# Kernel optimization log

Hardware: AMD Instinct MI355X
Metric: run time of the kernel (lower is better)

The kernel has to match this reference:

```python
import jax, jax.numpy as jnp
import numpy as np

DIM = 1024; VOCAB = 32000; HEADS = 16; HEAD_DIM = DIM // HEADS
SEG = 128; NPT = 16; WIDTH = 128
THETA = 0.1; ETA = 0.9; ALPHA = 0.01; EPS = 1e-6  # neural-memory lr / momentum / weight-decay


def l2n(x):
    return x / (jnp.linalg.norm(x, axis=-1, keepdims=True) + EPS)


def mlp(p, x):
    # 2-layer memory MLP: dim -> width -> dim, SiLU
    W1, b1, W2, b2 = p
    return jax.nn.silu(x @ W1 + b1) @ W2 + b2


def setup_inputs() -> dict:
    key = jax.random.key(0)
    ks = jax.random.split(key, 12)
    g = lambda k, s: jax.random.normal(k, s, jnp.float32) * 0.02
    z = lambda n: jnp.zeros((n,), jnp.float32)
    return {
        "x": jax.random.randint(ks[0], (2, 512), 0, VOCAB),
        "embedding": g(ks[1], (VOCAB, DIM)),
        "persistent": g(ks[2], (NPT, DIM)),
        "Wq": g(ks[3], (DIM, DIM)), "bq": z(DIM),
        "Wk": g(ks[4], (DIM, DIM)), "bk": z(DIM),
        "Wv": g(ks[5], (DIM, DIM)), "bv": z(DIM),
        "attn_in_w": g(ks[6], (DIM, 3 * DIM)), "attn_in_b": z(3 * DIM),
        "attn_out_w": g(ks[7], (DIM, DIM)), "attn_out_b": z(DIM),
        "mW1": g(ks[8], (DIM, WIDTH)), "mb1": z(WIDTH),
        "mW2": g(ks[9], (WIDTH, DIM)), "mb2": z(DIM),
        "head_w": g(ks[10], (DIM, VOCAB)), "head_b": z(VOCAB),
    }


def reference(x, embedding, persistent, Wq, bq, Wk, bk, Wv, bv,
              attn_in_w, attn_in_b, attn_out_w, attn_out_b,
              mW1, mb1, mW2, mb2, head_w, head_b):
    B, N = x.shape
    x_emb = embedding[x]  # [B, N, D]
    pad = (-N) % SEG
    if pad:
        x_emb = jnp.pad(x_emb, ((0, 0), (0, pad), (0, 0)))
    S = x_emb.shape[1] // SEG
    segs = x_emb.reshape(B, S, SEG, DIM).transpose(1, 0, 2, 3)  # [S, B, L, D]

    T = NPT + 2 * SEG  # persistent + retrieved memory + segment tokens
    causal = jnp.triu(jnp.ones((T, T), bool), 1)

    def mha(xc):  # [B, T, D] -> [B, T, D], torch nn.MultiheadAttention math
        q, k, v = jnp.split(xc @ attn_in_w + attn_in_b, 3, axis=-1)
        split = lambda t: t.reshape(B, T, HEADS, HEAD_DIM).transpose(0, 2, 1, 3)
        q, k, v = split(q), split(k), split(v)
        scores = jnp.einsum('bhqd,bhkd->bhqk', q, k) / np.sqrt(HEAD_DIM).astype(np.float32)
        scores = jnp.where(causal, -jnp.inf, scores)
        out = jnp.einsum('bhqk,bhkd->bhqd', jax.nn.softmax(scores, axis=-1), v)
        return out.transpose(0, 2, 1, 3).reshape(B, T, DIM) @ attn_out_w + attn_out_b

    # per-sample memory params (leading B axis) + zero momentum
    params0 = tuple(jnp.broadcast_to(w, (B,) + w.shape) for w in (mW1, mb1, mW2, mb2))
    mom0 = tuple(jnp.zeros_like(p) for p in params0)

    def mem_loss(p, k, v):
        e = mlp(p, k) - v
        return jnp.sum(e * e)

    def tok_step(carry, tok):  # tok: [B, D] -- one test-time gradient step on memory
        p, m = carry
        k = jax.lax.stop_gradient(l2n(tok @ Wk + bk))  # stop_grad_k=True
        v = tok @ Wv + bv                               # stop_grad_v=False
        grads = jax.vmap(jax.grad(mem_loss))(p, k, v)
        m = jax.tree.map(lambda mm, g: ETA * mm - THETA * g, m, grads)
        p = jax.tree.map(lambda pp, mm: (1.0 - ALPHA) * pp + mm, p, m)
        return (p, m), None

    retrieve = jax.vmap(mlp)  # vmap over per-sample memory params

    def seg_step(carry, segment):  # segment: [B, L, D]
        p, m = carry
        h = retrieve(p, l2n(segment @ Wq + bq))
        combined = jnp.concatenate(
            [jnp.broadcast_to(persistent, (B, NPT, DIM)), h, segment], axis=1)
        seg_out = mha(combined)[:, -SEG:, :]
        (p, m), _ = jax.lax.scan(tok_step, (p, m), seg_out.transpose(1, 0, 2))
        mem_out = retrieve(p, l2n(seg_out @ Wq + bq))
        return (p, m), seg_out * mem_out

    _, outs = jax.lax.scan(seg_step, (params0, mom0), segs)  # outs: [S, B, L, D]
    full = outs.transpose(1, 0, 2, 3).reshape(B, S * SEG, DIM)[:, :N, :]
    return full @ head_w + head_b
```

## Files before the change

kernel.cpp:

```cpp
#include <hip/hip_runtime.h>
#include <math.h>

#define D_    1024
#define B_    2
#define N_    512
#define SEG_  128
#define NSEG_ 4
#define NPT_  16
#define T_    272
#define NH_   16
#define HD_   64
#define W_    128
#define V_    32000

#define THETA_ 0.1f
#define ETA_   0.9f
#define PDEC_  0.99f
#define EPSN_  1e-6f
#define NB2_  32
#define FSTR_ 32

typedef __bf16 bf16x8 __attribute__((ext_vector_type(8)));
typedef float  f32x4  __attribute__((ext_vector_type(4)));

static const size_t XEMB = 0;
static const size_t OUTS = XEMB + (size_t)B_*N_*D_;
static const size_t PW1  = OUTS + (size_t)B_*N_*D_;
static const size_t PB1  = PW1  + (size_t)B_*D_*W_;
static const size_t PW2T = PB1  + (size_t)B_*W_;
static const size_t PB2  = PW2T + (size_t)B_*D_*W_;
static const size_t MOM  = PB2  + (size_t)B_*D_;
static const size_t MW1  = MOM;
static const size_t MB1  = MW1  + (size_t)B_*D_*W_;
static const size_t MW2T = MB1  + (size_t)B_*W_;
static const size_t MB2  = MW2T + (size_t)B_*D_*W_;
static const size_t MOMSZ = (size_t)B_*(D_*W_ + W_ + D_*W_ + D_);
static const size_t Q1   = MOM  + MOMSZ;
static const size_t AH   = Q1   + (size_t)B_*SEG_*D_;
static const size_t HBUF = AH   + (size_t)B_*SEG_*W_;
static const size_t COMB = HBUF + (size_t)B_*SEG_*D_;
static const size_t QKV  = COMB + (size_t)B_*T_*D_;
static const size_t ATTN = QKV  + (size_t)B_*T_*3*D_;
static const size_t SEGO = ATTN + (size_t)B_*SEG_*D_;
static const size_t KM   = SEGO + (size_t)B_*SEG_*D_;
static const size_t VM   = KM   + (size_t)B_*SEG_*D_;
static const size_t MEMO = VM   + (size_t)B_*SEG_*D_;
static const size_t WSEND = MEMO + (size_t)B_*SEG_*D_;

static const size_t AQ1K  = QKV;
static const size_t AQ1KM = AQ1K  + 32768;
static const size_t AGRAM = AQ1KM + 32768;
static const size_t ADZ1  = AGRAM + 32768;
static const size_t AA1H  = ADZ1  + 32768;
static const size_t AEH   = AA1H  + 32768;
static const size_t AEXR  = AEH + (size_t)B_*SEG_*D_;
static const size_t AEXEE = AEXR + 16384;
static const size_t COEF  = WSEND;
static const size_t ZEROB = COEF + 512;
static const size_t CBAR  = ZEROB + 128;

__device__ __forceinline__ float sigf(float x) { return 1.f/(1.f+expf(-x)); }

__device__ __forceinline__ void gstore(float* p, float v) {
  __hip_atomic_store(p, v, __ATOMIC_RELAXED, __HIP_MEMORY_SCOPE_AGENT);
}
__device__ __forceinline__ float gload(const float* p) {
  return __hip_atomic_load(p, __ATOMIC_RELAXED, __HIP_MEMORY_SCOPE_AGENT);
}

__device__ __forceinline__ void bsplit(float a, short& h, short& l) {
  unsigned u = __builtin_bit_cast(unsigned, a);
  unsigned hb = (u + 0x7fffu + ((u >> 16) & 1u)) >> 16;
  h = (short)hb;
  float hf = __builtin_bit_cast(float, hb << 16);
  float r = a - hf;
  unsigned ur = __builtin_bit_cast(unsigned, r);
  unsigned lb = (ur + 0x7fffu + ((ur >> 16) & 1u)) >> 16;
  l = (short)lb;
}

template<int BT, int SILU>
__global__ __launch_bounds__(256) void k_gemm(
    const float* __restrict__ A, const float* __restrict__ Bm,
    const float* __restrict__ bias, float* __restrict__ C,
    int M, int N, int K, long sA, long sB, long sC, long sBias)
{
  __shared__ float As[16][68];
  __shared__ float Bs[16][68];
  int bz = blockIdx.z;
  A += bz*sA; Bm += bz*sB; C += bz*sC; bias += bz*sBias;
  int n0 = blockIdx.x*64, m0 = blockIdx.y*64;
  int tid = threadIdx.x;
  int tx = tid & 15, ty = tid >> 4;
  int r  = tid >> 2;
  int kq = (tid & 3) * 4;
  float acc[4][4] = {};
  for (int k0 = 0; k0 < K; k0 += 16) {
    {
      int row = m0 + r;
      float4 v = make_float4(0.f,0.f,0.f,0.f);
      if (row < M) v = *(const float4*)(A + (long)row*K + k0 + kq);
      As[kq+0][r]=v.x; As[kq+1][r]=v.y; As[kq+2][r]=v.z; As[kq+3][r]=v.w;
    }
    if (BT) {
      int row = n0 + r;
      float4 v = *(const float4*)(Bm + (long)row*K + k0 + kq);
      Bs[kq+0][r]=v.x; Bs[kq+1][r]=v.y; Bs[kq+2][r]=v.z; Bs[kq+3][r]=v.w;
    } else {
      int c = tid & 63, r4 = tid >> 6;
      #pragma unroll
      for (int p = 0; p < 4; p++) {
        int kk = r4 + p*4;
        Bs[kk][c] = Bm[(long)(k0+kk)*N + n0 + c];
      }
    }
    __syncthreads();
    #pragma unroll
    for (int kk = 0; kk < 16; kk++) {
      float av[4], bv[4];
      #pragma unroll
      for (int i=0;i<4;i++) av[i] = As[kk][ty*4+i];
      #pragma unroll
      for (int j=0;j<4;j++) bv[j] = Bs[kk][tx*4+j];
      #pragma unroll
      for (int i=0;i<4;i++)
        #pragma unroll
        for (int j=0;j<4;j++)
          acc[i][j] = fmaf(av[i], bv[j], acc[i][j]);
    }
    __syncthreads();
  }
  #pragma unroll
  for (int i=0;i<4;i++) {
    int row = m0 + ty*4 + i;
    if (row >= M) continue;
    #pragma unroll
    for (int j=0;j<4;j++) {
      int col = n0 + tx*4 + j;
      float v = acc[i][j] + bias[col];
      if (SILU) v = v * sigf(v);
      C[(long)row*N + col] = v;
    }
  }
}

__global__ __launch_bounds__(256) void k_gemm2(
    const float* __restrict__ A, const float* __restrict__ B1,
    const float* __restrict__ B2, float* __restrict__ C1, float* __restrict__ C2,
    int K, long sA, long sB, long sC)
{
  __shared__ float As[16][68];
  __shared__ float B1s[16][68];
  __shared__ float B2s[16][68];
  int bz = blockIdx.z;
  A += bz*sA; B1 += bz*sB; B2 += bz*sB; C1 += bz*sC; C2 += bz*sC;
  int n0 = blockIdx.x*64, m0 = blockIdx.y*64;
  int tid = threadIdx.x;
  int tx = tid & 15, ty = tid >> 4;
  int r  = tid >> 2;
  int kq = (tid & 3) * 4;
  float acc1[4][4] = {}, acc2[4][4] = {};
  for (int k0 = 0; k0 < K; k0 += 16) {
    {
      float4 v = *(const float4*)(A + (long)(m0+r)*K + k0 + kq);
      As[kq+0][r]=v.x; As[kq+1][r]=v.y; As[kq+2][r]=v.z; As[kq+3][r]=v.w;
    }
    {
      int c = tid & 63, r4 = tid >> 6;
      #pragma unroll
      for (int p = 0; p < 4; p++) {
        int kk = r4 + p*4;
        B1s[kk][c] = B1[(long)(k0+kk)*W_ + n0 + c];
        B2s[kk][c] = B2[(long)(k0+kk)*W_ + n0 + c];
      }
    }
    __syncthreads();
    #pragma unroll
    for (int kk = 0; kk < 16; kk++) {
      float av[4], b1v[4], b2v[4];
      #pragma unroll
      for (int i=0;i<4;i++) av[i] = As[kk][ty*4+i];
      #pragma unroll
      for (int j=0;j<4;j++) { b1v[j] = B1s[kk][tx*4+j]; b2v[j] = B2s[kk][tx*4+j]; }
      #pragma unroll
      for (int i=0;i<4;i++)
        #pragma unroll
        for (int j=0;j<4;j++) {
          acc1[i][j] = fmaf(av[i], b1v[j], acc1[i][j]);
          acc2[i][j] = fmaf(av[i], b2v[j], acc2[i][j]);
        }
    }
    __syncthreads();
  }
  #pragma unroll
  for (int i=0;i<4;i++) {
    int row = m0 + ty*4 + i;
    #pragma unroll
    for (int j=0;j<4;j++) {
      int col = n0 + tx*4 + j;
      C1[(long)row*W_ + col] = acc1[i][j];
      C2[(long)row*W_ + col] = acc2[i][j];
    }
  }
}

__global__ __launch_bounds__(256) void k_gemm128(
    const float* __restrict__ A, const float* __restrict__ Bm,
    const float* __restrict__ bias, float* __restrict__ C,
    int M, int N, int K)
{
  __shared__ float As[16][132];
  __shared__ float Bs[16][132];
  int n0 = blockIdx.x*128, m0 = blockIdx.y*128;
  int tid = threadIdx.x;
  int tx = tid & 15, ty = tid >> 4;
  int ar = tid >> 1, ak = (tid & 1) * 8;
  int bk = tid >> 4, bn = (tid & 15) * 8;
  int arow = min(m0 + ar, M-1);
  float acc[8][8] = {};
  for (int k0 = 0; k0 < K; k0 += 16) {
    {
      const float* ap = A + (long)arow*K + k0 + ak;
      float4 v0 = *(const float4*)(ap);
      float4 v1 = *(const float4*)(ap+4);
      As[ak+0][ar]=v0.x; As[ak+1][ar]=v0.y; As[ak+2][ar]=v0.z; As[ak+3][ar]=v0.w;
      As[ak+4][ar]=v1.x; As[ak+5][ar]=v1.y; As[ak+6][ar]=v1.z; As[ak+7][ar]=v1.w;
      const float* bp = Bm + (long)(k0+bk)*N + n0 + bn;
      *(float4*)(&Bs[bk][bn])   = *(const float4*)(bp);
      *(float4*)(&Bs[bk][bn+4]) = *(const float4*)(bp+4);
    }
    __syncthreads();
    #pragma unroll
    for (int kk = 0; kk < 16; kk++) {
      float av[8], bv[8];
      #pragma unroll
      for (int i=0;i<8;i++) av[i] = As[kk][ty*8+i];
      #pragma unroll
      for (int j=0;j<8;j++) bv[j] = Bs[kk][tx*8+j];
      #pragma unroll
      for (int i=0;i<8;i++)
        #pragma unroll
        for (int j=0;j<8;j++)
          acc[i][j] = fmaf(av[i], bv[j], acc[i][j]);
    }
    __syncthreads();
  }
  #pragma unroll
  for (int i=0;i<8;i++) {
    int row = m0 + ty*8 + i;
    if (row >= M) continue;
    #pragma unroll
    for (int j=0;j<8;j++) acc[i][j] += bias[n0 + tx*8 + j];
    *(float4*)(C + (long)row*N + n0 + tx*8)     = make_float4(acc[i][0],acc[i][1],acc[i][2],acc[i][3]);
    *(float4*)(C + (long)row*N + n0 + tx*8 + 4) = make_float4(acc[i][4],acc[i][5],acc[i][6],acc[i][7]);
  }
}

__global__ __launch_bounds__(256) void k_head_mfma(
    const float* __restrict__ A, const float* __restrict__ Bm,
    const float* __restrict__ bias, float* __restrict__ C,
    int M, int N, int K)
{
  __shared__ short Ah[128][48];
  __shared__ short Al[128][48];
  __shared__ short Bh[32][132];
  __shared__ short Bl[32][132];
  int n0 = blockIdx.x*128, m0 = blockIdx.y*128;
  int tid = threadIdx.x;
  int wave = tid >> 6, lane = tid & 63;
  int wm = (wave >> 1) * 64, wn = (wave & 1) * 64;
  int lrow = lane & 15, lk = (lane >> 4) * 8;
  f32x4 acc[4][4] = {};
  for (int k0 = 0; k0 < K; k0 += 32) {
    __syncthreads();
    {
      int r = tid >> 1, kq = (tid & 1) * 16;
      const float* ap = A + (long)(m0 + r)*K + k0 + kq;
      #pragma unroll
      for (int q = 0; q < 16; q += 4) {
        float4 v = *(const float4*)(ap + q);
        short h0,l0,h1,l1,h2,l2,h3,l3;
        bsplit(v.x,h0,l0); bsplit(v.y,h1,l1); bsplit(v.z,h2,l2); bsplit(v.w,h3,l3);
        *(short4*)&Ah[r][kq+q] = make_short4(h0,h1,h2,h3);
        *(short4*)&Al[r][kq+q] = make_short4(l0,l1,l2,l3);
      }
    }
    {
      int kr = tid >> 3, nq = (tid & 7) * 16;
      const float* bp = Bm + (long)(k0 + kr)*N + n0 + nq;
      #pragma unroll
      for (int q = 0; q < 16; q += 4) {
        float4 v = *(const float4*)(bp + q);
        short h0,l0,h1,l1,h2,l2,h3,l3;
        bsplit(v.x,h0,l0); bsplit(v.y,h1,l1); bsplit(v.z,h2,l2); bsplit(v.w,h3,l3);
        *(short4*)&Bh[kr][nq+q] = make_short4(h0,h1,h2,h3);
        *(short4*)&Bl[kr][nq+q] = make_short4(l0,l1,l2,l3);
      }
    }
    __syncthreads();
    bf16x8 bh[4], bl[4];
    #pragma unroll
    for (int nf = 0; nf < 4; nf++) {
      int col = wn + nf*16 + lrow;
      #pragma unroll
      for (int j = 0; j < 8; j++) {
        bh[nf][j] = __builtin_bit_cast(__bf16, Bh[lk+j][col]);
        bl[nf][j] = __builtin_bit_cast(__bf16, Bl[lk+j][col]);
      }
    }
    #pragma unroll
    for (int mf = 0; mf < 4; mf++) {
      int arow2 = wm + mf*16 + lrow;
      bf16x8 ah = *(const bf16x8*)&Ah[arow2][lk];
      bf16x8 al = *(const bf16x8*)&Al[arow2][lk];
      #pragma unroll
      for (int nf = 0; nf < 4; nf++) {
        acc[mf][nf] = __builtin_amdgcn_mfma_f32_16x16x32_bf16(ah, bh[nf], acc[mf][nf], 0, 0, 0);
        acc[mf][nf] = __builtin_amdgcn_mfma_f32_16x16x32_bf16(ah, bl[nf], acc[mf][nf], 0, 0, 0);
        acc[mf][nf] = __builtin_amdgcn_mfma_f32_16x16x32_bf16(al, bh[nf], acc[mf][nf], 0, 0, 0);
      }
    }
  }
  #pragma unroll
  for (int mf = 0; mf < 4; mf++) {
    #pragma unroll
    for (int nf = 0; nf < 4; nf++) {
      int col = n0 + wn + nf*16 + lrow;
      float bv = bias[col];
      #pragma unroll
      for (int j = 0; j < 4; j++) {
        int row = m0 + wm + mf*16 + (lane >> 4)*4 + j;
        C[(long)row*N + col] = acc[mf][nf][j] + bv;
      }
    }
  }
}

__global__ void k_embed(const int* __restrict__ x, const float* __restrict__ emb,
                        float* __restrict__ xe)
{
  int row = blockIdx.x, tid = threadIdx.x;
  int idx = x[row];
  float4 v = *(const float4*)(emb + (long)idx*D_ + tid*4);
  *(float4*)(xe + (long)row*D_ + tid*4) = v;
}

#define PER_ 263296L
__global__ void k_init(const float* __restrict__ mW1in, const float* __restrict__ mb1in,
                       const float* __restrict__ mW2in, const float* __restrict__ mb2in,
                       float* __restrict__ pW1, float* __restrict__ pb1,
                       float* __restrict__ pW2T, float* __restrict__ pb2)
{
  long g = (long)blockIdx.x*256 + threadIdx.x;
  if (g >= 2*PER_) return;
  int b = (int)(g / PER_);
  long rr = g % PER_;
  if (rr < 131072)       pW1[(long)b*131072 + rr] = mW1in[rr];
  else if (rr < 131200)  pb1[b*W_ + (rr-131072)] = mb1in[rr-131072];
  else if (rr < 262272) { long l = rr-131200; int j=(int)(l>>7), h=(int)(l&127);
                          pW2T[(long)b*131072 + l] = mW2in[(long)h*D_ + j]; }
  else                   pb2[b*D_ + (rr-262272)] = mb2in[rr-262272];
}

__global__ void k_coef(float* __restrict__ c)
{
  if (blockIdx.x == 0 && threadIdx.x == 0) {
    c[0] = 1.f; c[128] = 1.f;
    float A = 1.f, eta_d = 1.f;
    for (int d = 1; d < 128; d++) {
      eta_d *= ETA_;
      A = PDEC_*A + eta_d;
      c[d] = A;
      c[128 + d] = eta_d;
    }
    c[256] = 1.f;
    float bp = 1.f;
    for (int t = 1; t <= 128; t++) { bp *= PDEC_; c[256 + t] = bp; }
  }
}

__global__ __launch_bounds__(256) void k_l2n(float* __restrict__ X)
{
  long row = blockIdx.x;
  float* p = X + row*D_;
  int tid = threadIdx.x;
  float4 v = *(float4*)(p + tid*4);
  float ss = v.x*v.x + v.y*v.y + v.z*v.z + v.w*v.w;
  for (int o=32;o;o>>=1) ss += __shfl_xor(ss,o);
  __shared__ float wsum[4];
  if ((tid&63)==0) wsum[tid>>6] = ss;
  __syncthreads();
  float tot = wsum[0]+wsum[1]+wsum[2]+wsum[3];
  float sc = 1.f/(sqrtf(tot)+EPSN_);
  v.x*=sc; v.y*=sc; v.z*=sc; v.w*=sc;
  *(float4*)(p + tid*4) = v;
}

__global__ void k_concat(const float* __restrict__ pers, const float* __restrict__ h,
                         const float* __restrict__ xemb, int s, float* __restrict__ comb)
{
  int row = blockIdx.x, b = blockIdx.y, tid = threadIdx.x;
  const float* src;
  if (row < NPT_)            src = pers + (long)row*D_;
  else if (row < NPT_+SEG_)  src = h    + ((long)b*SEG_ + (row-NPT_))*D_;
  else                       src = xemb + ((long)b*N_ + s*SEG_ + (row-NPT_-SEG_))*D_;
  float4 v = *(const float4*)(src + tid*4);
  *(float4*)(comb + ((long)b*T_ + row)*D_ + tid*4) = v;
}

__global__ __launch_bounds__(256) void k_attn(const float* __restrict__ qkv,
                                              float* __restrict__ outp)
{
  __shared__ float sQ[16][68];
  __shared__ float sKV[64][68];
  __shared__ float sS[16][273];
  int qt = blockIdx.x, head = blockIdx.y, b = blockIdx.z;
  int tid = threadIdx.x;
  const float* base = qkv + (long)b*T_*3*D_;
  int qoff = head*HD_, koff = D_ + head*HD_, voff = 2*D_ + head*HD_;
  int qrow0 = NPT_ + SEG_ + qt*16;
  {
    int rr = tid>>4, c4 = (tid&15)*4;
    float4 v = *(const float4*)(base + (long)(qrow0+rr)*3*D_ + qoff + c4);
    sQ[rr][c4]=v.x; sQ[rr][c4+1]=v.y; sQ[rr][c4+2]=v.z; sQ[rr][c4+3]=v.w;
  }
  __syncthreads();
  for (int j0 = 0; j0 < T_; j0 += 64) {
    int chunk = min(64, T_ - j0);
    {
      int jj = tid>>2, cq = (tid&3)*16;
      if (jj < chunk) {
        #pragma unroll
        for (int q4=0;q4<4;q4++) {
          float4 v = *(const float4*)(base + (long)(j0+jj)*3*D_ + koff + cq + q4*4);
          sKV[jj][cq+q4*4]=v.x; sKV[jj][cq+q4*4+1]=v.y; sKV[jj][cq+q4*4+2]=v.z; sKV[jj][cq+q4*4+3]=v.w;
        }
      }
    }
    __syncthreads();
    int rr = tid>>4, jj0 = tid&15;
    #pragma unroll
    for (int p=0;p<4;p++) {
      int jj = jj0 + p*16;
      if (jj < chunk) {
        float s = 0.f;
        #pragma unroll 8
        for (int c=0;c<HD_;c++) s = fmaf(sQ[rr][c], sKV[jj][c], s);
        s *= 0.125f;
        int jg = j0 + jj, qg = qrow0 + rr;
        if (jg > qg) s = -3.0e38f;
        sS[rr][jg] = s;
      }
    }
    __syncthreads();
  }
  {
    int rr = tid>>4, l16 = tid&15;
    float m = -3.4e38f;
    for (int j=l16; j<T_; j+=16) m = fmaxf(m, sS[rr][j]);
    for (int o=8;o;o>>=1) m = fmaxf(m, __shfl_xor(m,o));
    float sum = 0.f;
    for (int j=l16; j<T_; j+=16) { float e = expf(sS[rr][j]-m); sS[rr][j] = e; sum += e; }
    for (int o=8;o;o>>=1) sum += __shfl_xor(sum,o);
    float inv = 1.f/sum;
    for (int j=l16; j<T_; j+=16) sS[rr][j] *= inv;
  }
  __syncthreads();
  float acc[4] = {0.f,0.f,0.f,0.f};
  int rr = tid>>4, c4 = (tid&15)*4;
  for (int j0 = 0; j0 < T_; j0 += 64) {
    int chunk = min(64, T_ - j0);
    {
      int jj = tid>>2, cq = (tid&3)*16;
      if (jj < chunk) {
        #pragma unroll
        for (int q4=0;q4<4;q4++) {
          float4 v = *(const float4*)(base + (long)(j0+jj)*3*D_ + voff + cq + q4*4);
          sKV[jj][cq+q4*4]=v.x; sKV[jj][cq+q4*4+1]=v.y; sKV[jj][cq+q4*4+2]=v.z; sKV[jj][cq+q4*4+3]=v.w;
        }
      }
    }
    __syncthreads();
    for (int jj=0; jj<chunk; jj++) {
      float p = sS[rr][j0+jj];
      #pragma unroll
      for (int i=0;i<4;i++) acc[i] = fmaf(p, sKV[jj][c4+i], acc[i]);
    }
    __syncthreads();
  }
  float4 o4 = make_float4(acc[0],acc[1],acc[2],acc[3]);
  *(float4*)(outp + ((long)(b*SEG_) + qt*16 + rr)*D_ + head*HD_ + c4) = o4;
}

__device__ __forceinline__ void gbar(int* flags, int blk, int gen)
{
  asm volatile("s_waitcnt vmcnt(0) lgkmcnt(0)" ::: "memory");
  __syncthreads();
  if (threadIdx.x == 0)
    __hip_atomic_store(flags + blk*FSTR_, gen, __ATOMIC_RELAXED, __HIP_MEMORY_SCOPE_AGENT);
  if (threadIdx.x < NB2_) {
    while (__hip_atomic_load(flags + threadIdx.x*FSTR_, __ATOMIC_RELAXED,
                             __HIP_MEMORY_SCOPE_AGENT) < gen)
      __builtin_amdgcn_s_sleep(1);
  }
  __syncthreads();
}

__global__ __launch_bounds__(256) void k_scan(
  const float* __restrict__ pW2T, const float* __restrict__ mW2T,
  float* __restrict__ pb1, float* __restrict__ mb1,
  float* __restrict__ pb2, float* __restrict__ mb2,
  const float* __restrict__ Vm,
  const float* __restrict__ q1k, const float* __restrict__ q1km,
  const float* __restrict__ G,
  float* __restrict__ dz1o, float* __restrict__ a1o, float* __restrict__ eo,
  float* __restrict__ exR, float* __restrict__ exEE,
  const float* __restrict__ coef, int* __restrict__ barbase, int seg)
{
  __shared__ float sDZ[128][129];
  __shared__ float sA1[128][129];
  __shared__ float sEh[128][33];
  __shared__ float sB1[128], sMB1[128], sZ1[128], sR[128];
  __shared__ float sB2[32], sMB2[32];
  __shared__ float sAt[128];
  __shared__ float sBp[129];
  __shared__ float sGc[128];
  __shared__ float sS[128];
  __shared__ float sEEc[128];

  int b = blockIdx.y, blk = blockIdx.x, tid = threadIdx.x;
  int j0 = blk*32;
  int* flags = barbase + b*(NB2_*FSTR_);
  int gbase = seg*200;
  const float* W0 = pW2T + (long)b*131072;
  const float* Wm = mW2T + (long)b*131072;

  if (tid < 128) { sAt[tid] = coef[tid]; sB1[tid] = pb1[b*W_+tid]; sMB1[tid] = mb1[b*W_+tid]; }
  else if (tid < 160) { int j = tid-128; sB2[j] = pb2[b*D_+j0+j]; sMB2[j] = mb2[b*D_+j0+j]; }
  for (int i = tid; i < 129; i += 256) sBp[i] = coef[256+i];
  __syncthreads();

  for (int t = 0; t < SEG_; ++t) {
    int par = t & 1;
    float bp = sBp[t];
    float ca = (t>0) ? ETA_*sAt[t-1] : 0.f;

    float rq1k = 0.f, rq1km = 0.f;
    if (tid < 128) {
      rq1k  = q1k [((long)b*SEG_+t)*W_ + tid];
      rq1km = q1km[((long)b*SEG_+t)*W_ + tid];
      if (t > 0) {
        float mm = ETA_*sMB1[tid] - THETA_*sDZ[t-1][tid];
        sMB1[tid] = mm; sB1[tid] = PDEC_*sB1[tid] + mm;
      }
      if (tid < t) sGc[tid] = sAt[t-1-tid]*G[((long)b*SEG_+t)*SEG_ + tid];
    } else if (tid < 160) {
      int j = tid-128;
      if (t > 0) {
        float mm = ETA_*sMB2[j] - 2.f*THETA_*sEh[t-1][j];
        sMB2[j] = mm; sB2[j] = PDEC_*sB2[j] + mm;
      }
    }
    __syncthreads();

    if (tid < 128) {
      float acc = 0.f;
      for (int u = 0; u < t; ++u) acc = fmaf(sGc[u], sDZ[u][tid], acc);
      float z1 = bp*rq1k + ca*rq1km + sB1[tid] - THETA_*acc;
      sZ1[tid] = z1;
      sA1[t][tid] = z1 * sigf(z1);
    }
    __syncthreads();

    if (tid < t) {
      float acc = 0.f;
      #pragma unroll 8
      for (int h = 0; h < 128; ++h) acc = fmaf(sA1[tid][h], sA1[t][h], acc);
      sS[tid] = -2.f*THETA_*sAt[t-1-tid]*acc;
    }
    __syncthreads();

    {
      int j = tid >> 3, l = tid & 7;
      const float* w0r = W0 + (long)(j0+j)*128;
      const float* wmr = Wm + (long)(j0+j)*128;
      float g = 0.f, gm = 0.f;
      for (int h = l; h < 128; h += 8) {
        g  = fmaf(w0r[h], sA1[t][h], g);
        gm = fmaf(wmr[h], sA1[t][h], gm);
      }
      float corr = 0.f;
      for (int u = l; u < t; u += 8) corr = fmaf(sS[u], sEh[u][j], corr);
      float tot = bp*g + ca*gm + corr;
      tot += __shfl_xor(tot,4); tot += __shfl_xor(tot,2); tot += __shfl_xor(tot,1);
      if (l == 0) sEh[t][j] = tot + sB2[j] - Vm[((long)b*SEG_+t)*D_ + j0+j];
    }
    __syncthreads();

    {
      int h = tid >> 1, half = tid & 1;
      float racc = 0.f;
      for (int jj = half*16; jj < half*16+16; ++jj) {
        float w = bp*W0[(long)(j0+jj)*128 + h] + ca*Wm[(long)(j0+jj)*128 + h];
        racc = fmaf(w, sEh[t][jj], racc);
      }
      racc += __shfl_xor(racc,1);
      if (half == 0) gstore(&exR[(((long)par*B_ + b)*NB2_ + blk)*W_ + h], racc);
      if (h < t) {
        float eacc = 0.f;
        for (int jj = half*16; jj < half*16+16; ++jj)
          eacc = fmaf(sEh[h][jj], sEh[t][jj], eacc);
        eacc += __shfl_xor(eacc,1);
        if (half == 0) gstore(&exEE[(((long)par*B_ + b)*NB2_ + blk)*W_ + h], eacc);
      }
    }
    gbar(flags, blk, gbase + t + 1);

    {
      int h = tid >> 1, half = tid & 1;
      float racc = 0.f;
      #pragma unroll
      for (int k = 0; k < 16; ++k)
        racc += gload(&exR[(((long)par*B_ + b)*NB2_ + half*16 + k)*W_ + h]);
      racc += __shfl_xor(racc,1);
      if (half == 0) sR[h] = racc;
      if (h < t) {
        float eacc = 0.f;
        #pragma unroll
        for (int k = 0; k < 16; ++k)
          eacc += gload(&exEE[(((long)par*B_ + b)*NB2_ + half*16 + k)*W_ + h]);
        eacc += __shfl_xor(eacc,1);
        if (half == 0) sEEc[h] = -2.f*THETA_*sAt[t-1-h]*eacc;
      }
    }
    __syncthreads();
    if (tid < 128) {
      float macc = 0.f;
      for (int u = 0; u < t; ++u) macc = fmaf(sEEc[u], sA1[u][tid], macc);
      float z = sZ1[tid], sg = sigf(z);
      sDZ[t][tid] = 2.f*(sR[tid] + macc)*sg*(1.f + z*(1.f - sg));
    }
    __syncthreads();
  }

  if (tid < 128) {
    if (blk == 0) {
      float mm = ETA_*sMB1[tid] - THETA_*sDZ[127][tid];
      mb1[b*W_ + tid] = mm;
      pb1[b*W_ + tid] = PDEC_*sB1[tid] + mm;
    }
  } else if (tid < 160) {
    int j = tid-128;
    float mm = ETA_*sMB2[j] - 2.f*THETA_*sEh[127][j];
    mb2[b*D_ + j0+j] = mm;
    pb2[b*D_ + j0+j] = PDEC_*sB2[j] + mm;
  }
  for (int i = tid; i < 128*4; i += 256) {
    int t2 = i >> 2, hh = (i & 3) + blk*4;
    dz1o[((long)b*SEG_+t2)*W_ + hh] = sDZ[t2][hh];
    a1o [((long)b*SEG_+t2)*W_ + hh] = sA1[t2][hh];
  }
  for (int i = tid; i < 128*32; i += 256) {
    int t2 = i >> 5, jj = i & 31;
    eo[((long)b*SEG_+t2)*D_ + j0+jj] = sEh[t2][jj];
  }
}

__global__ __launch_bounds__(256) void k_recon(
  float* __restrict__ pW1, float* __restrict__ mW1,
  float* __restrict__ pW2T, float* __restrict__ mW2T,
  const float* __restrict__ KMp, const float* __restrict__ Eh,
  const float* __restrict__ DZ1, const float* __restrict__ A1h,
  const float* __restrict__ coef)
{
  __shared__ float s1[16][33];
  __shared__ float s2[16][65];
  __shared__ float sCA[128], sCE[128];
  int dt = blockIdx.x, ht = blockIdx.y, kb = blockIdx.z;
  int kind = kb >> 1, b = kb & 1;
  int tid = threadIdx.x;
  int d0 = dt*32, hb = ht*64;
  const float* in1 = (kind ? Eh : KMp) + (long)b*SEG_*D_;
  const float* in2 = (kind ? A1h : DZ1) + (long)b*SEG_*W_;
  float* Pb = (kind ? pW2T : pW1) + (long)b*131072;
  float* Mb = (kind ? mW2T : mW1) + (long)b*131072;
  float f = kind ? -2.f*THETA_ : -THETA_;
  if (tid < 128) {
    sCA[tid] = f*coef[127 - tid];
    sCE[tid] = f*coef[128 + 127 - tid];
  }
  __syncthreads();
  int dd = tid >> 3, le = tid & 7;
  float accP[8] = {}, accM[8] = {};
  for (int u0 = 0; u0 < 128; u0 += 16) {
    for (int i = tid; i < 16*32; i += 256) {
      int uu = i >> 5, d2 = i & 31;
      s1[uu][d2] = in1[(long)(u0+uu)*D_ + d0 + d2];
    }
    for (int i = tid; i < 16*64; i += 256) {
      int uu = i >> 6, hl = i & 63;
      s2[uu][hl] = in2[(long)(u0+uu)*W_ + hb + hl];
    }
    __syncthreads();
    #pragma unroll
    for (int uu = 0; uu < 16; uu++) {
      float a = s1[uu][dd];
      float cAu = sCA[u0+uu], cEu = sCE[u0+uu];
      #pragma unroll
      for (int k = 0; k < 8; k++) {
        float v = a * s2[uu][k*8 + le];
        accP[k] = fmaf(cAu, v, accP[k]);
        accM[k] = fmaf(cEu, v, accM[k]);
      }
    }
    __syncthreads();
  }
  float b128 = coef[256 + 128];
  float eA   = ETA_*coef[127];
  float e128 = ETA_*coef[128 + 127];
  #pragma unroll
  for (int k = 0; k < 8; k++) {
    long idx = (long)(d0+dd)*W_ + hb + k*8 + le;
    float Po = Pb[idx], Mo = Mb[idx];
    Pb[idx] = b128*Po + eA*Mo + accP[k];
    Mb[idx] = e128*Mo + accM[k];
  }
}

__global__ __launch_bounds__(256) void k_gemmkvq(
    const float* __restrict__ A,
    const float* __restrict__ Wk, const float* __restrict__ bk,
    const float* __restrict__ Wv, const float* __restrict__ bv,
    const float* __restrict__ Wq, const float* __restrict__ bq,
    float* __restrict__ KMo, float* __restrict__ VMo, float* __restrict__ Q1o)
{
  __shared__ float As[16][132];
  __shared__ float Bs[16][132];
  int bx = blockIdx.x;
  int sel = bx >> 3;
  int c0 = (bx & 7) * 128;
  int m0 = blockIdx.y * 128;
  const float* Bm   = sel == 0 ? Wk : sel == 1 ? Wv : Wq;
  const float* bias = sel == 0 ? bk : sel == 1 ? bv : bq;
  float* C          = sel == 0 ? KMo : sel == 1 ? VMo : Q1o;
  int tid = threadIdx.x;
  int tx = tid & 15, ty = tid >> 4;
  int ar = tid >> 1, ak = (tid & 1) * 8;
  int bkr = tid >> 4, bn = (tid & 15) * 8;
  float acc[8][8] = {};
  for (int k0 = 0; k0 < D_; k0 += 16) {
    {
      const float* ap = A + (long)(m0+ar)*D_ + k0 + ak;
      float4 v0 = *(const float4*)(ap);
      float4 v1 = *(const float4*)(ap+4);
      As[ak+0][ar]=v0.x; As[ak+1][ar]=v0.y; As[ak+2][ar]=v0.z; As[ak+3][ar]=v0.w;
      As[ak+4][ar]=v1.x; As[ak+5][ar]=v1.y; As[ak+6][ar]=v1.z; As[ak+7][ar]=v1.w;
      const float* bp = Bm + (long)(k0+bkr)*D_ + c0 + bn;
      *(float4*)(&Bs[bkr][bn])   = *(const float4*)(bp);
      *(float4*)(&Bs[bkr][bn+4]) = *(const float4*)(bp+4);
    }
    __syncthreads();
    #pragma unroll
    for (int kk = 0; kk < 16; kk++) {
      float av[8], bv8[8];
      #pragma unroll
      for (int i=0;i<8;i++) av[i] = As[kk][ty*8+i];
      #pragma unroll
      for (int j=0;j<8;j++) bv8[j] = Bs[kk][tx*8+j];
      #pragma unroll
      for (int i=0;i<8;i++)
        #pragma unroll
        for (int j=0;j<8;j++)
          acc[i][j] = fmaf(av[i], bv8[j], acc[i][j]);
    }
    __syncthreads();
  }
  #pragma unroll
  for (int i=0;i<8;i++) {
    int row = m0 + ty*8 + i;
    #pragma unroll
    for (int j=0;j<8;j++) acc[i][j] += bias[c0 + tx*8 + j];
    *(float4*)(C + (long)row*D_ + c0 + tx*8)     = make_float4(acc[i][0],acc[i][1],acc[i][2],acc[i][3]);
    *(float4*)(C + (long)row*D_ + c0 + tx*8 + 4) = make_float4(acc[i][4],acc[i][5],acc[i][6],acc[i][7]);
  }
}

__global__ void k_mul(const float* __restrict__ so, const float* __restrict__ mo,
                      float* __restrict__ outs, int s)
{
  int l = blockIdx.x, b = blockIdx.y, tid = threadIdx.x;
  long src = ((long)b*SEG_ + l)*D_ + tid*4;
  float4 a = *(const float4*)(so + src);
  float4 c = *(const float4*)(mo + src);
  a.x*=c.x; a.y*=c.y; a.z*=c.z; a.w*=c.w;
  *(float4*)(outs + ((long)b*N_ + s*SEG_ + l)*D_ + tid*4) = a;
}

static inline void gemm(const float* A, const float* Bm, const float* bias, float* C,
                        int M, int N, int K, long sA, long sB, long sC, long sBias,
                        int batch, int bt, int silu_, hipStream_t st)
{
  dim3 g(N/64, (M+63)/64, batch), blk(256);
  if (!bt && !silu_) k_gemm<0,0><<<g,blk,0,st>>>(A,Bm,bias,C,M,N,K,sA,sB,sC,sBias);
  else if (!bt && silu_) k_gemm<0,1><<<g,blk,0,st>>>(A,Bm,bias,C,M,N,K,sA,sB,sC,sBias);
  else k_gemm<1,0><<<g,blk,0,st>>>(A,Bm,bias,C,M,N,K,sA,sB,sC,sBias);
}

extern "C" void kernel_launch(void* const* d_in, const int* in_sizes, int n_in,
                              void* d_out, int out_size, void* d_ws, size_t ws_size,
                              hipStream_t stream)
{
  (void)in_sizes; (void)n_in; (void)out_size; (void)ws_size;
  const int*   x     = (const int*)  d_in[0];
  const float* emb   = (const float*)d_in[1];
  const float* pers  = (const float*)d_in[2];
  const float* Wq    = (const float*)d_in[3];
  const float* bq    = (const float*)d_in[4];
  const float* Wk    = (const float*)d_in[5];
  const float* bk    = (const float*)d_in[6];
  const float* Wv    = (const float*)d_in[7];
  const float* bv    = (const float*)d_in[8];
  const float* aiw   = (const float*)d_in[9];
  const float* aib   = (const float*)d_in[10];
  const float* aow   = (const float*)d_in[11];
  const float* aob   = (const float*)d_in[12];
  const float* mW1in = (const float*)d_in[13];
  const float* mb1in = (const float*)d_in[14];
  const float* mW2in = (const float*)d_in[15];
  const float* mb2in = (const float*)d_in[16];
  const float* headw = (const float*)d_in[17];
  const float* headb = (const float*)d_in[18];
  float* out = (float*)d_out;
  float* ws  = (float*)d_ws;

  hipMemsetAsync(ws + MOM, 0, MOMSZ*sizeof(float), stream);
  hipMemsetAsync(ws + ZEROB, 0, 128*sizeof(float), stream);
  hipMemsetAsync(ws + CBAR, 0, (size_t)B_*NB2_*FSTR_*sizeof(int), stream);
  k_embed<<<dim3(B_*N_), dim3(256), 0, stream>>>(x, emb, ws+XEMB);
  k_init<<<dim3((2*PER_+255)/256), dim3(256), 0, stream>>>(
      mW1in, mb1in, mW2in, mb2in, ws+PW1, ws+PB1, ws+PW2T, ws+PB2);
  k_coef<<<dim3(1), dim3(64), 0, stream>>>(ws+COEF);

  for (int s = 0; s < NSEG_; s++) {
    const float* segA = ws + XEMB + (size_t)s*SEG_*D_;
    gemm(segA, Wq, bq, ws+Q1, SEG_, D_, D_, (long)N_*D_, 0, (long)SEG_*D_, 0, B_, 0, 0, stream);
    k_l2n<<<dim3(B_*SEG_), dim3(256), 0, stream>>>(ws+Q1);
    gemm(ws+Q1, ws+PW1, ws+PB1, ws+AH, SEG_, W_, D_, (long)SEG_*D_, (long)D_*W_, (long)SEG_*W_, W_, B_, 0, 1, stream);
    gemm(ws+AH, ws+PW2T, ws+PB2, ws+HBUF, SEG_, D_, W_, (long)SEG_*W_, (long)D_*W_, (long)SEG_*D_, D_, B_, 1, 0, stream);
    k_concat<<<dim3(T_, B_), dim3(256), 0, stream>>>(pers, ws+HBUF, ws+XEMB, s, ws+COMB);
    k_gemm128<<<dim3(3*D_/128, (B_*T_+127)/128), dim3(256), 0, stream>>>(
        ws+COMB, aiw, aib, ws+QKV, B_*T_, 3*D_, D_);
    k_attn<<<dim3(8, NH_, B_), dim3(256), 0, stream>>>(ws+QKV, ws+ATTN);
    gemm(ws+ATTN, aow, aob, ws+SEGO, B_*SEG_, D_, D_, 0, 0, 0, 0, 1, 0, 0, stream);
    k_gemmkvq<<<dim3(24, 2), dim3(256), 0, stream>>>(
        ws+SEGO, Wk, bk, Wv, bv, Wq, bq, ws+KM, ws+VM, ws+Q1);
    k_l2n<<<dim3(B_*SEG_), dim3(256), 0, stream>>>(ws+KM);
    k_l2n<<<dim3(B_*SEG_), dim3(256), 0, stream>>>(ws+Q1);
    k_gemm2<<<dim3(2, 2, B_), dim3(256), 0, stream>>>(
        ws+KM, ws+PW1, ws+MW1, ws+AQ1K, ws+AQ1KM,
        D_, (long)SEG_*D_, (long)D_*W_, (long)SEG_*W_);
    gemm(ws+KM, ws+KM,  ws+ZEROB, ws+AGRAM, SEG_, SEG_, D_, (long)SEG_*D_, (long)SEG_*D_, (long)SEG_*SEG_, 0, B_, 1, 0, stream);
    k_scan<<<dim3(NB2_, B_), dim3(256), 0, stream>>>(
        ws+PW2T, ws+MW2T, ws+PB1, ws+MB1, ws+PB2, ws+MB2, ws+VM,
        ws+AQ1K, ws+AQ1KM, ws+AGRAM,
        ws+ADZ1, ws+AA1H, ws+AEH,
        ws+AEXR, ws+AEXEE,
        ws+COEF, (int*)(ws+CBAR), s);
    k_recon<<<dim3(32, 2, 4), dim3(256), 0, stream>>>(
        ws+PW1, ws+MW1, ws+PW2T, ws+MW2T,
        ws+KM, ws+AEH, ws+ADZ1, ws+AA1H, ws+COEF);
    gemm(ws+Q1, ws+PW1, ws+PB1, ws+AH, SEG_, W_, D_, (long)SEG_*D_, (long)D_*W_, (long)SEG_*W_, W_, B_, 0, 1, stream);
    gemm(ws+AH, ws+PW2T, ws+PB2, ws+MEMO, SEG_, D_, W_, (long)SEG_*W_, (long)D_*W_, (long)SEG_*D_, D_, B_, 1, 0, stream);
    k_mul<<<dim3(SEG_, B_), dim3(256), 0, stream>>>(ws+SEGO, ws+MEMO, ws+OUTS, s);
  }
  k_head_mfma<<<dim3(V_/128, (B_*N_)/128), dim3(256), 0, stream>>>(
      ws+OUTS, headw, headb, out, B_*N_, V_, D_);
}
```

Before: 8.503 ms.

## Move dense projections to split-bf16 MFMA and cache scan weights in registers

Replaces the FP32 SIMT tiled GEMMs for the Wq projection, QKV in-projection, attention out-projection and fused K/V/Q projection with a bf16 MFMA kernel. Each FP32 operand is split into high and low bf16 parts and three MFMA products are accumulated to stay close to FP32 accuracy. The sequential per-token scan kernel now preloads its slice of the W2 parameter and momentum rows into registers once, instead of re-reading them from global memory on every token step. The split-bf16 path trades some precision and extra MFMA work for matrix-core throughput, and the register cache raises register pressure in the scan kernel.

New measurement: 7.426 ms. -12.7%, faster.

```diff
diff --git a/kernel.cpp b/kernel.cpp
--- a/kernel.cpp
+++ b/kernel.cpp
@@ -204,55 +204,174 @@
   }
 }
 
-__global__ __launch_bounds__(256) void k_gemm128(
+__global__ __launch_bounds__(256) void k_gemm_mfma(
     const float* __restrict__ A, const float* __restrict__ Bm,
     const float* __restrict__ bias, float* __restrict__ C,
-    int M, int N, int K)
-{
-  __shared__ float As[16][132];
-  __shared__ float Bs[16][132];
+    int M, int N, int K, long sA, long sB, long sC, long sBias)
+{
+  __shared__ short Ah[128][48];
+  __shared__ short Al[128][48];
+  __shared__ short Bh[32][132];
+  __shared__ short Bl[32][132];
+  int bz = blockIdx.z;
+  A += bz*sA; Bm += bz*sB; C += bz*sC; bias += bz*sBias;
   int n0 = blockIdx.x*128, m0 = blockIdx.y*128;
   int tid = threadIdx.x;
-  int tx = tid & 15, ty = tid >> 4;
-  int ar = tid >> 1, ak = (tid & 1) * 8;
-  int bk = tid >> 4, bn = (tid & 15) * 8;
-  int arow = min(m0 + ar, M-1);
-  float acc[8][8] = {};
-  for (int k0 = 0; k0 < K; k0 += 16) {
-    {
-      const float* ap = A + (long)arow*K + k0 + ak;
-      float4 v0 = *(const float4*)(ap);
-      float4 v1 = *(const float4*)(ap+4);
-      As[ak+0][ar]=v0.x; As[ak+1][ar]=v0.y; As[ak+2][ar]=v0.z; As[ak+3][ar]=v0.w;
-      As[ak+4][ar]=v1.x; As[ak+5][ar]=v1.y; As[ak+6][ar]=v1.z; As[ak+7][ar]=v1.w;
-      const float* bp = Bm + (long)(k0+bk)*N + n0 + bn;
-      *(float4*)(&Bs[bk][bn])   = *(const float4*)(bp);
-      *(float4*)(&Bs[bk][bn+4]) = *(const float4*)(bp+4);
-    }
-    __syncthreads();
-    #pragma unroll
-    for (int kk = 0; kk < 16; kk++) {
-      float av[8], bv[8];
-      #pragma unroll
-      for (int i=0;i<8;i++) av[i] = As[kk][ty*8+i];
-      #pragma unroll
-      for (int j=0;j<8;j++) bv[j] = Bs[kk][tx*8+j];
-      #pragma unroll
-      for (int i=0;i<8;i++)
-        #pragma unroll
-        for (int j=0;j<8;j++)
-          acc[i][j] = fmaf(av[i], bv[j], acc[i][j]);
-    }
-    __syncthreads();
+  int wave = tid >> 6, lane = tid & 63;
+  int wm = (wave >> 1) * 64, wn = (wave & 1) * 64;
+  int lrow = lane & 15, lk = (lane >> 4) * 8;
+  int arow0 = min(m0 + (tid >> 1), M-1);
+  f32x4 acc[4][4] = {};
+  for (int k0 = 0; k0 < K; k0 += 32) {
+    __syncthreads();
+    {
+      int r = tid >> 1, kq = (tid & 1) * 16;
+      const float* ap = A + (long)arow0*K + k0 + kq;
+      #pragma unroll
+      for (int q = 0; q < 16; q += 4) {
+        float4 v = *(const float4*)(ap + q);
+        short h0,l0,h1,l1,h2,l2,h3,l3;
+        bsplit(v.x,h0,l0); bsplit(v.y,h1,l1); bsplit(v.z,h2,l2); bsplit(v.w,h3,l3);
+        *(short4*)&Ah[r][kq+q] = make_short4(h0,h1,h2,h3);
+        *(short4*)&Al[r][kq+q] = make_short4(l0,l1,l2,l3);
+      }
+    }
+    {
+      int kr = tid >> 3, nq = (tid & 7) * 16;
+      const float* bp = Bm + (long)(k0 + kr)*N + n0 + nq;
+      #pragma unroll
+      for (int q = 0; q < 16; q += 4) {
+        float4 v = *(const float4*)(bp + q);
+        short h0,l0,h1,l1,h2,l2,h3,l3;
+        bsplit(v.x,h0,l0); bsplit(v.y,h1,l1); bsplit(v.z,h2,l2); bsplit(v.w,h3,l3);
+        *(short4*)&Bh[kr][nq+q] = make_short4(h0,h1,h2,h3);
+        *(short4*)&Bl[kr][nq+q] = make_short4(l0,l1,l2,l3);
+      }
+    }
+    __syncthreads();
+    bf16x8 bh[4], bl[4];
+    #pragma unroll
+    for (int nf = 0; nf < 4; nf++) {
+      int col = wn + nf*16 + lrow;
+      #pragma unroll
+      for (int j = 0; j < 8; j++) {
+        bh[nf][j] = __builtin_bit_cast(__bf16, Bh[lk+j][col]);
+        bl[nf][j] = __builtin_bit_cast(__bf16, Bl[lk+j][col]);
+      }
+    }
+    #pragma unroll
+    for (int mf = 0; mf < 4; mf++) {
+      int ar2 = wm + mf*16 + lrow;
+      bf16x8 ah = *(const bf16x8*)&Ah[ar2][lk];
+      bf16x8 al = *(const bf16x8*)&Al[ar2][lk];
+      #pragma unroll
+      for (int nf = 0; nf < 4; nf++) {
+        acc[mf][nf] = __builtin_amdgcn_mfma_f32_16x16x32_bf16(ah, bh[nf], acc[mf][nf], 0, 0, 0);
+        acc[mf][nf] = __builtin_amdgcn_mfma_f32_16x16x32_bf16(ah, bl[nf], acc[mf][nf], 0, 0, 0);
+        acc[mf][nf] = __builtin_amdgcn_mfma_f32_16x16x32_bf16(al, bh[nf], acc[mf][nf], 0, 0, 0);
+      }
+    }
   }
   #pragma unroll
-  for (int i=0;i<8;i++) {
-    int row = m0 + ty*8 + i;
-    if (row >= M) continue;
-    #pragma unroll
-    for (int j=0;j<8;j++) acc[i][j] += bias[n0 + tx*8 + j];
-    *(float4*)(C + (long)row*N + n0 + tx*8)     = make_float4(acc[i][0],acc[i][1],acc[i][2],acc[i][3]);
-    *(float4*)(C + (long)row*N + n0 + tx*8 + 4) = make_float4(acc[i][4],acc[i][5],acc[i][6],acc[i][7]);
+  for (int mf = 0; mf < 4; mf++) {
+    #pragma unroll
+    for (int nf = 0; nf < 4; nf++) {
+      int col = n0 + wn + nf*16 + lrow;
+      float bv = bias[col];
+      #pragma unroll
+      for (int j = 0; j < 4; j++) {
+        int row = m0 + wm + mf*16 + (lane >> 4)*4 + j;
+        if (row < M) C[(long)row*N + col] = acc[mf][nf][j] + bv;
+      }
+    }
+  }
+}
+
+__global__ __launch_bounds__(256) void k_gemmkvq_m(
+    const float* __restrict__ A,
+    const float* __restrict__ Wk, const float* __restrict__ bk,
+    const float* __restrict__ Wv, const float* __restrict__ bv,
+    const float* __restrict__ Wq, const float* __restrict__ bq,
+    float* __restrict__ KMo, float* __restrict__ VMo, float* __restrict__ Q1o)
+{
+  __shared__ short Ah[128][48];
+  __shared__ short Al[128][48];
+  __shared__ short Bh[32][132];
+  __shared__ short Bl[32][132];
+  int bx = blockIdx.x;
+  int sel = bx >> 3;
+  int n0 = (bx & 7) * 128;
+  int m0 = blockIdx.y * 128;
+  const float* Bm   = sel == 0 ? Wk : sel == 1 ? Wv : Wq;
+  const float* bias = sel == 0 ? bk : sel == 1 ? bv : bq;
+  float* C          = sel == 0 ? KMo : sel == 1 ? VMo : Q1o;
+  int tid = threadIdx.x;
+  int wave = tid >> 6, lane = tid & 63;
+  int wm = (wave >> 1) * 64, wn = (wave & 1) * 64;
+  int lrow = lane & 15, lk = (lane >> 4) * 8;
+  f32x4 acc[4][4] = {};
+  for (int k0 = 0; k0 < D_; k0 += 32) {
+    __syncthreads();
+    {
+      int r = tid >> 1, kq = (tid & 1) * 16;
+      const float* ap = A + (long)(m0 + r)*D_ + k0 + kq;
+      #pragma unroll
+      for (int q = 0; q < 16; q += 4) {
+        float4 v = *(const float4*)(ap + q);
+        short h0,l0,h1,l1,h2,l2,h3,l3;
+        bsplit(v.x,h0,l0); bsplit(v.y,h1,l1); bsplit(v.z,h2,l2); bsplit(v.w,h3,l3);
+        *(short4*)&Ah[r][kq+q] = make_short4(h0,h1,h2,h3);
+        *(short4*)&Al[r][kq+q] = make_short4(l0,l1,l2,l3);
+      }
+    }
+    {
+      int kr = tid >> 3, nq = (tid & 7) * 16;
+      const float* bp = Bm + (long)(k0 + kr)*D_ + n0 + nq;
+      #pragma unroll
+      for (int q = 0; q < 16; q += 4) {
+        float4 v = *(const float4*)(bp + q);
+        short h0,l0,h1,l1,h2,l2,h3,l3;
+        bsplit(v.x,h0,l0); bsplit(v.y,h1,l1); bsplit(v.z,h2,l2); bsplit(v.w,h3,l3);
+        *(short4*)&Bh[kr][nq+q] = make_short4(h0,h1,h2,h3);
+        *(short4*)&Bl[kr][nq+q] = make_short4(l0,l1,l2,l3);
+      }
+    }
+    __syncthreads();
+    bf16x8 bh[4], bl[4];
+    #pragma unroll
+    for (int nf = 0; nf < 4; nf++) {
+      int col = wn + nf*16 + lrow;
+      #pragma unroll
+      for (int j = 0; j < 8; j++) {
+        bh[nf][j] = __builtin_bit_cast(__bf16, Bh[lk+j][col]);
+        bl[nf][j] = __builtin_bit_cast(__bf16, Bl[lk+j][col]);
+      }
+    }
+    #pragma unroll
+    for (int mf = 0; mf < 4; mf++) {
+      int ar2 = wm + mf*16 + lrow;
+      bf16x8 ah = *(const bf16x8*)&Ah[ar2][lk];
+      bf16x8 al = *(const bf16x8*)&Al[ar2][lk];
+      #pragma unroll
+      for (int nf = 0; nf < 4; nf++) {
+        acc[mf][nf] = __builtin_amdgcn_mfma_f32_16x16x32_bf16(ah, bh[nf], acc[mf][nf], 0, 0, 0);
+        acc[mf][nf] = __builtin_amdgcn_mfma_f32_16x16x32_bf16(ah, bl[nf], acc[mf][nf], 0, 0, 0);
+        acc[mf][nf] = __builtin_amdgcn_mfma_f32_16x16x32_bf16(al, bh[nf], acc[mf][nf], 0, 0, 0);
+      }
+    }
+  }
+  #pragma unroll
+  for (int mf = 0; mf < 4; mf++) {
+    #pragma unroll
+    for (int nf = 0; nf < 4; nf++) {
+      int col = n0 + wn + nf*16 + lrow;
+      float bvx = bias[col];
+      #pragma unroll
+      for (int j = 0; j < 4; j++) {
+        int row = m0 + wm + mf*16 + (lane >> 4)*4 + j;
+        C[(long)row*D_ + col] = acc[mf][nf][j] + bvx;
+      }
+    }
   }
 }
 
@@ -535,6 +654,21 @@
   const float* W0 = pW2T + (long)b*131072;
   const float* Wm = mW2T + (long)b*131072;
 
+  int jD = tid >> 3, lD = tid & 7;
+  float rD0[16], rDm[16];
+  #pragma unroll
+  for (int k = 0; k < 16; k++) {
+    rD0[k] = W0[(long)(j0+jD)*128 + lD + 8*k];
+    rDm[k] = Wm[(long)(j0+jD)*128 + lD + 8*k];
+  }
+  int hE = tid >> 1, halfE = tid & 1;
+  float rE0[16], rEm[16];
+  #pragma unroll
+  for (int q = 0; q < 16; q++) {
+    rE0[q] = W0[(long)(j0 + halfE*16 + q)*128 + hE];
+    rEm[q] = Wm[(long)(j0 + halfE*16 + q)*128 + hE];
+  }
+
   if (tid < 128) { sAt[tid] = coef[tid]; sB1[tid] = pb1[b*W_+tid]; sMB1[tid] = mb1[b*W_+tid]; }
   else if (tid < 160) { int j = tid-128; sB2[j] = pb2[b*D_+j0+j]; sMB2[j] = mb2[b*D_+j0+j]; }
   for (int i = tid; i < 129; i += 256) sBp[i] = coef[256+i];
@@ -581,56 +715,55 @@
     __syncthreads();
 
     {
-      int j = tid >> 3, l = tid & 7;
-      const float* w0r = W0 + (long)(j0+j)*128;
-      const float* wmr = Wm + (long)(j0+j)*128;
       float g = 0.f, gm = 0.f;
-      for (int h = l; h < 128; h += 8) {
-        g  = fmaf(w0r[h], sA1[t][h], g);
-        gm = fmaf(wmr[h], sA1[t][h], gm);
+      #pragma unroll
+      for (int k = 0; k < 16; k++) {
+        float a = sA1[t][lD + 8*k];
+        g  = fmaf(rD0[k], a, g);
+        gm = fmaf(rDm[k], a, gm);
       }
       float corr = 0.f;
-      for (int u = l; u < t; u += 8) corr = fmaf(sS[u], sEh[u][j], corr);
+      for (int u = lD; u < t; u += 8) corr = fmaf(sS[u], sEh[u][jD], corr);
       float tot = bp*g + ca*gm + corr;
       tot += __shfl_xor(tot,4); tot += __shfl_xor(tot,2); tot += __shfl_xor(tot,1);
-      if (l == 0) sEh[t][j] = tot + sB2[j] - Vm[((long)b*SEG_+t)*D_ + j0+j];
-    }
-    __syncthreads();
-
-    {
-      int h = tid >> 1, half = tid & 1;
+      if (lD == 0) sEh[t][jD] = tot + sB2[jD] - Vm[((long)b*SEG_+t)*D_ + j0+jD];
+    }
+    __syncthreads();
+
+    {
       float racc = 0.f;
-      for (int jj = half*16; jj < half*16+16; ++jj) {
-        float w = bp*W0[(long)(j0+jj)*128 + h] + ca*Wm[(long)(j0+jj)*128 + h];
-        racc = fmaf(w, sEh[t][jj], racc);
+      #pragma unroll
+      for (int q = 0; q < 16; ++q) {
+        float w = bp*rE0[q] + ca*rEm[q];
+        racc = fmaf(w, sEh[t][halfE*16 + q], racc);
       }
       racc += __shfl_xor(racc,1);
-      if (half == 0) gstore(&exR[(((long)par*B_ + b)*NB2_ + blk)*W_ + h], racc);
-      if (h < t) {
+      if (halfE == 0) gstore(&exR[(((long)par*B_ + b)*NB2_ + blk)*W_ + hE], racc);
+      if (hE < t) {
         float eacc = 0.f;
-        for (int jj = half*16; jj < half*16+16; ++jj)
-          eacc = fmaf(sEh[h][jj], sEh[t][jj], eacc);
+        #pragma unroll
+        for (int q = 0; q < 16; ++q)
+          eacc = fmaf(sEh[hE][halfE*16 + q], sEh[t][halfE*16 + q], eacc);
         eacc += __shfl_xor(eacc,1);
-        if (half == 0) gstore(&exEE[(((long)par*B_ + b)*NB2_ + blk)*W_ + h], eacc);
+        if (halfE == 0) gstore(&exEE[(((long)par*B_ + b)*NB2_ + blk)*W_ + hE], eacc);
       }
     }
     gbar(flags, blk, gbase + t + 1);
 
     {
-      int h = tid >> 1, half = tid & 1;
       float racc = 0.f;
       #pragma unroll
       for (int k = 0; k < 16; ++k)
-        racc += gload(&exR[(((long)par*B_ + b)*NB2_ + half*16 + k)*W_ + h]);
+        racc += gload(&exR[(((long)par*B_ + b)*NB2_ + halfE*16 + k)*W_ + hE]);
       racc += __shfl_xor(racc,1);
-      if (half == 0) sR[h] = racc;
-      if (h < t) {
+      if (halfE == 0) sR[hE] = racc;
+      if (hE < t) {
         float eacc = 0.f;
         #pragma unroll
         for (int k = 0; k < 16; ++k)
-          eacc += gload(&exEE[(((long)par*B_ + b)*NB2_ + half*16 + k)*W_ + h]);
+          eacc += gload(&exEE[(((long)par*B_ + b)*NB2_ + halfE*16 + k)*W_ + hE]);
         eacc += __shfl_xor(eacc,1);
-        if (half == 0) sEEc[h] = -2.f*THETA_*sAt[t-1-h]*eacc;
+        if (halfE == 0) sEEc[hE] = -2.f*THETA_*sAt[t-1-hE]*eacc;
       }
     }
     __syncthreads();
@@ -724,64 +857,6 @@
     float Po = Pb[idx], Mo = Mb[idx];
     Pb[idx] = b128*Po + eA*Mo + accP[k];
     Mb[idx] = e128*Mo + accM[k];
-  }
-}
-
-__global__ __launch_bounds__(256) void k_gemmkvq(
-    const float* __restrict__ A,
-    const float* __restrict__ Wk, const float* __restrict__ bk,
-    const float* __restrict__ Wv, const float* __restrict__ bv,
-    const float* __restrict__ Wq, const float* __restrict__ bq,
-    float* __restrict__ KMo, float* __restrict__ VMo, float* __restrict__ Q1o)
-{
-  __shared__ float As[16][132];
-  __shared__ float Bs[16][132];
-  int bx = blockIdx.x;
-  int sel = bx >> 3;
-  int c0 = (bx & 7) * 128;
-  int m0 = blockIdx.y * 128;
-  const float* Bm   = sel == 0 ? Wk : sel == 1 ? Wv : Wq;
-  const float* bias = sel == 0 ? bk : sel == 1 ? bv : bq;
-  float* C          = sel == 0 ? KMo : sel == 1 ? VMo : Q1o;
-  int tid = threadIdx.x;
-  int tx = tid & 15, ty = tid >> 4;
-  int ar = tid >> 1, ak = (tid & 1) * 8;
-  int bkr = tid >> 4, bn = (tid & 15) * 8;
-  float acc[8][8] = {};
-  for (int k0 = 0; k0 < D_; k0 += 16) {
-    {
-      const float* ap = A + (long)(m0+ar)*D_ + k0 + ak;
-      float4 v0 = *(const float4*)(ap);
-      float4 v1 = *(const float4*)(ap+4);
-      As[ak+0][ar]=v0.x; As[ak+1][ar]=v0.y; As[ak+2][ar]=v0.z; As[ak+3][ar]=v0.w;
-      As[ak+4][ar]=v1.x; As[ak+5][ar]=v1.y; As[ak+6][ar]=v1.z; As[ak+7][ar]=v1.w;
-      const float* bp = Bm + (long)(k0+bkr)*D_ + c0 + bn;
-      *(float4*)(&Bs[bkr][bn])   = *(const float4*)(bp);
-      *(float4*)(&Bs[bkr][bn+4]) = *(const float4*)(bp+4);
-    }
-    __syncthreads();
-    #pragma unroll
-    for (int kk = 0; kk < 16; kk++) {
-      float av[8], bv8[8];
-      #pragma unroll
-      for (int i=0;i<8;i++) av[i] = As[kk][ty*8+i];
-      #pragma unroll
-      for (int j=0;j<8;j++) bv8[j] = Bs[kk][tx*8+j];
-      #pragma unroll
-      for (int i=0;i<8;i++)
-        #pragma unroll
-        for (int j=0;j<8;j++)
-          acc[i][j] = fmaf(av[i], bv8[j], acc[i][j]);
-    }
-    __syncthreads();
-  }
-  #pragma unroll
-  for (int i=0;i<8;i++) {
-    int row = m0 + ty*8 + i;
-    #pragma unroll
-    for (int j=0;j<8;j++) acc[i][j] += bias[c0 + tx*8 + j];
-    *(float4*)(C + (long)row*D_ + c0 + tx*8)     = make_float4(acc[i][0],acc[i][1],acc[i][2],acc[i][3]);
-    *(float4*)(C + (long)row*D_ + c0 + tx*8 + 4) = make_float4(acc[i][4],acc[i][5],acc[i][6],acc[i][7]);
   }
 }
 
@@ -843,16 +918,18 @@
 
   for (int s = 0; s < NSEG_; s++) {
     const float* segA = ws + XEMB + (size_t)s*SEG_*D_;
-    gemm(segA, Wq, bq, ws+Q1, SEG_, D_, D_, (long)N_*D_, 0, (long)SEG_*D_, 0, B_, 0, 0, stream);
+    k_gemm_mfma<<<dim3(8, 1, B_), dim3(256), 0, stream>>>(
+        segA, Wq, bq, ws+Q1, SEG_, D_, D_, (long)N_*D_, 0, (long)SEG_*D_, 0);
     k_l2n<<<dim3(B_*SEG_), dim3(256), 0, stream>>>(ws+Q1);
     gemm(ws+Q1, ws+PW1, ws+PB1, ws+AH, SEG_, W_, D_, (long)SEG_*D_, (long)D_*W_, (long)SEG_*W_, W_, B_, 0, 1, stream);
     gemm(ws+AH, ws+PW2T, ws+PB2, ws+HBUF, SEG_, D_, W_, (long)SEG_*W_, (long)D_*W_, (long)SEG_*D_, D_, B_, 1, 0, stream);
     k_concat<<<dim3(T_, B_), dim3(256), 0, stream>>>(pers, ws+HBUF, ws+XEMB, s, ws+COMB);
-    k_gemm128<<<dim3(3*D_/128, (B_*T_+127)/128), dim3(256), 0, stream>>>(
-        ws+COMB, aiw, aib, ws+QKV, B_*T_, 3*D_, D_);
+    k_gemm_mfma<<<dim3(3*D_/128, (B_*T_+127)/128, 1), dim3(256), 0, stream>>>(
+        ws+COMB, aiw, aib, ws+QKV, B_*T_, 3*D_, D_, 0, 0, 0, 0);
     k_attn<<<dim3(8, NH_, B_), dim3(256), 0, stream>>>(ws+QKV, ws+ATTN);
-    gemm(ws+ATTN, aow, aob, ws+SEGO, B_*SEG_, D_, D_, 0, 0, 0, 0, 1, 0, 0, stream);
-    k_gemmkvq<<<dim3(24, 2), dim3(256), 0, stream>>>(
+    k_gemm_mfma<<<dim3(D_/128, 2, 1), dim3(256), 0, stream>>>(
+        ws+ATTN, aow, aob, ws+SEGO, B_*SEG_, D_, D_, 0, 0, 0, 0);
+    k_gemmkvq_m<<<dim3(24, 2), dim3(256), 0, stream>>>(
         ws+SEGO, Wk, bk, Wv, bv, Wq, bq, ws+KM, ws+VM, ws+Q1);
     k_l2n<<<dim3(B_*SEG_), dim3(256), 0, stream>>>(ws+KM);
     k_l2n<<<dim3(B_*SEG_), dim3(256), 0, stream>>>(ws+Q1);
```
